# Optimization experiments

Hardware: AMD Instinct MI355X
Metric: run time of the kernel (lower is better)

The kernel has to match this reference:

```python
import jax, jax.numpy as jnp
import numpy as np

B, N, M, C, H = 256, 4096, 64, 512, 4
IN, OUT = 64, 64
EPS = 1e-8

def setup_inputs():
    key = jax.random.key(0)
    ks = jax.random.split(key, 8)
    def w(k, shape, scale=0.05):
        return jax.random.normal(k, shape, dtype=jnp.float32) * scale
    return {
        "in_data": jax.random.normal(ks[0], (B, IN), dtype=jnp.float32),
        "memory": jax.random.normal(ks[1], (B, N, M), dtype=jnp.float32),
        "h0": jnp.zeros((B, C), jnp.float32),
        "c0": jnp.zeros((B, C), jnp.float32),
        "prev_weights": jnp.zeros((2 * H, B, N), jnp.float32),
        "prev_reads": jax.random.normal(ks[2], (H, B, M), dtype=jnp.float32),
        "W_ih": w(ks[3], (4 * C, IN + H * M)),
        "b_ih": jnp.zeros((4 * C,), jnp.float32),
        "W_hh": w(ks[4], (4 * C, C)),
        "b_hh": jnp.zeros((4 * C,), jnp.float32),
        "W_out": w(ks[5], (OUT, C + H * M)),
        "b_out": jnp.zeros((OUT,), jnp.float32),
        "W_addr": w(ks[6], (2 * H, M + 6, C)),
        "b_addr": jnp.zeros((2 * H, M + 6), jnp.float32),
        "W_ea": w(ks[7], (H, 2 * M, C)),
        "b_ea": jnp.zeros((H, 2 * M), jnp.float32),
    }


def reference(in_data, memory, h0, c0, prev_weights, prev_reads,
              W_ih, b_ih, W_hh, b_hh, W_out, b_out,
              W_addr, b_addr, W_ea, b_ea):
    # ---- controller: LSTMCell over [input, prev_reads...] ----
    x = jnp.concatenate([in_data] + [prev_reads[i] for i in range(H)], axis=-1)  # [B, IN+H*M]
    gates = x @ W_ih.T + b_ih + h0 @ W_hh.T + b_hh                               # [B, 4C]
    i_g, f_g, g_g, o_g = jnp.split(gates, 4, axis=-1)
    c = jax.nn.sigmoid(f_g) * c0 + jax.nn.sigmoid(i_g) * jnp.tanh(g_g)
    h = jax.nn.sigmoid(o_g) * jnp.tanh(c)

    # ---- heads: alternate read / write, sequential over memory ----
    mem = memory
    reads = []
    for hi in range(2 * H):
        p = c @ W_addr[hi].T + b_addr[hi]                     # [B, M+6]
        k = jnp.tanh(p[:, :M])                                # key
        beta = jax.nn.softplus(p[:, M:M + 1])                 # key strength
        gate = jax.nn.sigmoid(p[:, M + 1:M + 2])              # interpolation gate
        s = jax.nn.softmax(p[:, M + 2:M + 5], axis=-1)        # shift weights (3)
        gamma = 1.0 + jax.nn.softplus(p[:, M + 5:M + 6])      # sharpening
        # content addressing: cosine similarity against all memory rows
        dot = jnp.einsum('bnm,bm->bn', mem, k)                # [B, N]
        norms = jnp.linalg.norm(mem, axis=-1) * jnp.linalg.norm(k, axis=-1, keepdims=True)
        wc = jax.nn.softmax(beta * dot / (norms + EPS), axis=-1)
        # interpolation with previous weights
        wg = gate * wc + (1.0 - gate) * prev_weights[hi]
        # circular shift convolution (shifts -1, 0, +1)
        ws = (s[:, 0:1] * jnp.roll(wg, 1, axis=-1)
              + s[:, 1:2] * wg
              + s[:, 2:3] * jnp.roll(wg, -1, axis=-1))
        # sharpening
        wp = ws ** gamma
        w = wp / (jnp.sum(wp, axis=-1, keepdims=True) + EPS)
        if hi % 2 == 0:  # read head
            reads.append(jnp.einsum('bn,bnm->bm', w, mem))
        else:            # write head: erase then add
            ea = c @ W_ea[hi // 2].T + b_ea[hi // 2]          # [B, 2M]
            e = jax.nn.sigmoid(ea[:, :M])
            a = jnp.tanh(ea[:, M:])
            mem = mem * (1.0 - w[:, :, None] * e[:, None, :]) + w[:, :, None] * a[:, None, :]

    # ---- output layer over [h, reads...] ----
    state = jnp.concatenate([h] + reads, axis=-1)             # [B, C+H*M]
    return jax.nn.sigmoid(state @ W_out.T + b_out)            # [B, OUT]
```

## Files before the change

kernel.cpp:

```cpp
#include <hip/hip_runtime.h>
#include <math.h>

#define EPSF 1e-8f

__device__ __forceinline__ float sigf(float x) { return 1.0f / (1.0f + expf(-x)); }
__device__ __forceinline__ float softplusf(float x) { return x > 20.0f ? x : log1pf(expf(x)); }

__global__ void pack_x_kernel(const float* __restrict__ in_data,
                              const float* __restrict__ prev_reads,
                              const float* __restrict__ h0,
                              float* __restrict__ X) {
  int idx = blockIdx.x * 256 + threadIdx.x;
  if (idx >= 256 * 832) return;
  int b = idx / 832, t = idx % 832;
  float v;
  if (t < 64) v = in_data[b * 64 + t];
  else if (t < 320) { int i = (t - 64) >> 6, m = (t - 64) & 63; v = prev_reads[((size_t)i * 256 + b) * 64 + m]; }
  else v = h0[b * 512 + (t - 320)];
  X[idx] = v;
}

__global__ __launch_bounds__(256) void gemm_gates_kernel(
    const float* __restrict__ X, const float* __restrict__ W_ih,
    const float* __restrict__ W_hh, const float* __restrict__ b_ih,
    const float* __restrict__ b_hh, float* __restrict__ gates) {
  __shared__ float As[16][33];
  __shared__ float Ws[16][65];
  int tid = threadIdx.x, tx = tid & 15, ty = tid >> 4;
  int row0 = blockIdx.y * 32, col0 = blockIdx.x * 64;
  float acc[2][4] = {{0,0,0,0},{0,0,0,0}};
  for (int k0 = 0; k0 < 832; k0 += 16) {
    const float* Wp; int kw, KW;
    if (k0 < 320) { Wp = W_ih; kw = k0; KW = 320; }
    else          { Wp = W_hh; kw = k0 - 320; KW = 512; }
    for (int i = tid; i < 32 * 16; i += 256) {
      int rr = i >> 4, cc = i & 15;
      As[cc][rr] = X[(size_t)(row0 + rr) * 832 + k0 + cc];
    }
    for (int i = tid; i < 64 * 16; i += 256) {
      int rr = i >> 4, cc = i & 15;
      Ws[cc][rr] = Wp[(size_t)(col0 + rr) * KW + kw + cc];
    }
    __syncthreads();
#pragma unroll
    for (int kk = 0; kk < 16; kk++) {
      float a0 = As[kk][ty * 2 + 0], a1 = As[kk][ty * 2 + 1];
      float w0 = Ws[kk][tx * 4 + 0], w1 = Ws[kk][tx * 4 + 1];
      float w2 = Ws[kk][tx * 4 + 2], w3 = Ws[kk][tx * 4 + 3];
      acc[0][0] += a0 * w0; acc[0][1] += a0 * w1; acc[0][2] += a0 * w2; acc[0][3] += a0 * w3;
      acc[1][0] += a1 * w0; acc[1][1] += a1 * w1; acc[1][2] += a1 * w2; acc[1][3] += a1 * w3;
    }
    __syncthreads();
  }
  for (int i = 0; i < 2; i++)
    for (int j = 0; j < 4; j++) {
      int cc = col0 + tx * 4 + j;
      gates[(size_t)(row0 + ty * 2 + i) * 2048 + cc] = acc[i][j] + b_ih[cc] + b_hh[cc];
    }
}

__global__ void lstm_elem_kernel(const float* __restrict__ gates,
                                 const float* __restrict__ c0,
                                 float* __restrict__ c, float* __restrict__ h) {
  int idx = blockIdx.x * 256 + threadIdx.x;
  if (idx >= 256 * 512) return;
  int b = idx >> 9, u = idx & 511;
  const float* g = gates + (size_t)b * 2048;
  float ig = sigf(g[u]), fg = sigf(g[512 + u]);
  float gg = tanhf(g[1024 + u]), og = sigf(g[1536 + u]);
  float cv = fg * c0[idx] + ig * gg;
  c[idx] = cv;
  h[idx] = og * tanhf(cv);
}

__global__ __launch_bounds__(256) void gemm_heads_kernel(
    const float* __restrict__ C, const float* __restrict__ W_addr,
    const float* __restrict__ W_ea, const float* __restrict__ b_addr,
    const float* __restrict__ b_ea, float* __restrict__ p_raw) {
  __shared__ float As[16][33];
  __shared__ float Ws[16][65];
  int tid = threadIdx.x, tx = tid & 15, ty = tid >> 4;
  int row0 = blockIdx.y * 32, col0 = blockIdx.x * 64;
  float acc[2][4] = {{0,0,0,0},{0,0,0,0}};
  for (int k0 = 0; k0 < 512; k0 += 16) {
    for (int i = tid; i < 32 * 16; i += 256) {
      int rr = i >> 4, cc = i & 15;
      As[cc][rr] = C[(size_t)(row0 + rr) * 512 + k0 + cc];
    }
    for (int i = tid; i < 64 * 16; i += 256) {
      int rr = i >> 4, cc = i & 15;
      int col = col0 + rr;
      float v = 0.f;
      if (col < 560) v = W_addr[(size_t)col * 512 + k0 + cc];
      else if (col < 1072) v = W_ea[(size_t)(col - 560) * 512 + k0 + cc];
      Ws[cc][rr] = v;
    }
    __syncthreads();
#pragma unroll
    for (int kk = 0; kk < 16; kk++) {
      float a0 = As[kk][ty * 2 + 0], a1 = As[kk][ty * 2 + 1];
      float w0 = Ws[kk][tx * 4 + 0], w1 = Ws[kk][tx * 4 + 1];
      float w2 = Ws[kk][tx * 4 + 2], w3 = Ws[kk][tx * 4 + 3];
      acc[0][0] += a0 * w0; acc[0][1] += a0 * w1; acc[0][2] += a0 * w2; acc[0][3] += a0 * w3;
      acc[1][0] += a1 * w0; acc[1][1] += a1 * w1; acc[1][2] += a1 * w2; acc[1][3] += a1 * w3;
    }
    __syncthreads();
  }
  for (int i = 0; i < 2; i++)
    for (int j = 0; j < 4; j++) {
      int col = col0 + tx * 4 + j;
      if (col < 1072) {
        float bias = col < 560 ? b_addr[col] : b_ea[col - 560];
        p_raw[(size_t)(row0 + ty * 2 + i) * 1072 + col] = acc[i][j] + bias;
      }
    }
}

__global__ void head_params_kernel(const float* __restrict__ p_raw,
    float* __restrict__ kvec, float* __restrict__ knorm,
    float* __restrict__ betav, float* __restrict__ gatev,
    float* __restrict__ sv, float* __restrict__ gammav,
    float* __restrict__ evec, float* __restrict__ avec) {
  int hi = blockIdx.x, b = blockIdx.y, t = threadIdx.x;
  const float* p = p_raw + (size_t)b * 1072 + hi * 70;
  if (t < 64) {
    float kvv = tanhf(p[t]);
    kvec[((size_t)hi * 256 + b) * 64 + t] = kvv;
    float s = kvv * kvv;
    for (int m = 1; m < 64; m <<= 1) s += __shfl_xor(s, m);
    if (t == 0) {
      int hb = hi * 256 + b;
      knorm[hb] = sqrtf(s);
      betav[hb] = softplusf(p[64]);
      gatev[hb] = sigf(p[65]);
      float a0 = p[66], a1 = p[67], a2 = p[68];
      float mm = fmaxf(a0, fmaxf(a1, a2));
      float e0 = expf(a0 - mm), e1 = expf(a1 - mm), e2 = expf(a2 - mm);
      float es = e0 + e1 + e2;
      sv[hb * 3 + 0] = e0 / es; sv[hb * 3 + 1] = e1 / es; sv[hb * 3 + 2] = e2 / es;
      gammav[hb] = 1.0f + softplusf(p[69]);
    }
  } else if ((hi & 1) && hi < 7) {
    int wj = hi >> 1, t2 = t - 64;
    const float* ea = p_raw + (size_t)b * 1072 + 560 + wj * 128;
    evec[((size_t)wj * 256 + b) * 64 + t2] = sigf(ea[t2]);
    avec[((size_t)wj * 256 + b) * 64 + t2] = tanhf(ea[64 + t2]);
  }
}

template<int NW, int NKEYS, int READ_MODE>
__global__ __launch_bounds__(256) void pass_kernel(
    const float* __restrict__ mem, const float* __restrict__ kvec,
    int keyA, int keyB, const float* __restrict__ w_all,
    const float* __restrict__ evec, const float* __restrict__ avec,
    int rw_head, float* __restrict__ dot_a, float* __restrict__ dot_b,
    float* __restrict__ normr, float* __restrict__ read_out) {
  const int BB = 256, NN = 4096;
  int b = blockIdx.y;
  int n0 = blockIdx.x * 256;
  int tid = threadIdx.x;
  int wv = tid >> 6, lane = tid & 63;
  int q = lane & 15, r = lane >> 4;
  size_t bo = (size_t)b * NN;

  float4 kA = make_float4(0,0,0,0), kB = make_float4(0,0,0,0);
  if (NKEYS >= 1) kA = *(const float4*)(kvec + ((size_t)keyA * BB + b) * 64 + q * 4);
  if (NKEYS >= 2) kB = *(const float4*)(kvec + ((size_t)keyB * BB + b) * 64 + q * 4);
  float4 ev[3], av[3];
  const float* wrow[3];
  const int whead[3] = {1, 3, 5};
#pragma unroll
  for (int j = 0; j < NW; j++) {
    ev[j] = *(const float4*)(evec + ((size_t)j * BB + b) * 64 + q * 4);
    av[j] = *(const float4*)(avec + ((size_t)j * BB + b) * 64 + q * 4);
    wrow[j] = w_all + ((size_t)whead[j] * BB + b) * NN;
  }
  const float* rwrow = READ_MODE ? (w_all + ((size_t)rw_head * BB + b) * NN) : nullptr;

  __shared__ float sdA[256], sdB[256], snm[256];
  __shared__ float sred[4][16][4];

  const float4* m4 = (const float4*)mem;
  size_t base = (bo + n0 + (size_t)wv * 64) * 16 + lane;

  float rx = 0.f, ry = 0.f, rz = 0.f, rw_ = 0.f;
#pragma unroll 4
  for (int t = 0; t < 16; t++) {
    int nl = wv * 64 + t * 4 + r;
    int n = n0 + nl;
    float4 v = m4[base + (size_t)t * 64];
    float vx = v.x, vy = v.y, vz = v.z, vw = v.w;
#pragma unroll
    for (int j = 0; j < NW; j++) {
      if (READ_MODE == 1 && j == NW - 1) {
        float rwt = rwrow[n];
        rx += rwt * vx; ry += rwt * vy; rz += rwt * vz; rw_ += rwt * vw;
      }
      float wj = wrow[j][n];
      vx = vx * (1.f - wj * ev[j].x) + wj * av[j].x;
      vy = vy * (1.f - wj * ev[j].y) + wj * av[j].y;
      vz = vz * (1.f - wj * ev[j].z) + wj * av[j].z;
      vw = vw * (1.f - wj * ev[j].w) + wj * av[j].w;
    }
    if (READ_MODE == 2) {
      float rwt = rwrow[n];
      rx += rwt * vx; ry += rwt * vy; rz += rwt * vz; rw_ += rwt * vw;
    }
    if (NKEYS >= 1) {
      float dA = vx * kA.x + vy * kA.y + vz * kA.z + vw * kA.w;
      float nm = vx * vx + vy * vy + vz * vz + vw * vw;
      float dB = 0.f;
      if (NKEYS >= 2) dB = vx * kB.x + vy * kB.y + vz * kB.z + vw * kB.w;
#pragma unroll
      for (int m = 1; m < 16; m <<= 1) {
        dA += __shfl_xor(dA, m);
        nm += __shfl_xor(nm, m);
        if (NKEYS >= 2) dB += __shfl_xor(dB, m);
      }
      if (q == 0) {
        sdA[nl] = dA; snm[nl] = sqrtf(nm);
        if (NKEYS >= 2) sdB[nl] = dB;
      }
    }
  }
  if (READ_MODE) {
#pragma unroll
    for (int m = 16; m < 64; m <<= 1) {
      rx += __shfl_xor(rx, m); ry += __shfl_xor(ry, m);
      rz += __shfl_xor(rz, m); rw_ += __shfl_xor(rw_, m);
    }
    if (r == 0) { sred[wv][q][0] = rx; sred[wv][q][1] = ry; sred[wv][q][2] = rz; sred[wv][q][3] = rw_; }
  }
  __syncthreads();
  if (NKEYS >= 1) {
    dot_a[bo + n0 + tid] = sdA[tid];
    normr[bo + n0 + tid] = snm[tid];
    if (NKEYS >= 2) dot_b[bo + n0 + tid] = sdB[tid];
  }
  if (READ_MODE && tid < 64) {
    int qq = tid >> 2, cc = tid & 3;
    float s = sred[0][qq][cc] + sred[1][qq][cc] + sred[2][qq][cc] + sred[3][qq][cc];
    atomicAdd(&read_out[b * 64 + qq * 4 + cc], s);
  }
}

__global__ __launch_bounds__(256) void chain_kernel(
    const float* __restrict__ dot_a, const float* __restrict__ dot_b,
    const float* __restrict__ normr, const float* __restrict__ knorm,
    const float* __restrict__ betav, const float* __restrict__ gatev,
    const float* __restrict__ sv, const float* __restrict__ gammav,
    const float* __restrict__ prev_w, float* __restrict__ w_all,
    int head_base) {
  const int NN = 4096, BB = 256;
  int which = blockIdx.x, b = blockIdx.y;
  int head = head_base + which;
  const float* dp = which ? dot_b : dot_a;
  size_t bo = (size_t)b * NN;
  __shared__ float wg[4096];
  __shared__ float redm[4], reds[4], reds2[4];
  int tid = threadIdx.x;
  int lane = tid & 63, wv = tid >> 6;
  int hb = head * BB + b;
  float kn = knorm[hb], be = betav[hb], ga = gatev[hb], gm = gammav[hb];
  float s0 = sv[hb * 3 + 0], s1 = sv[hb * 3 + 1], s2 = sv[hb * 3 + 2];

  float sc[16];
  float mx = -1e30f;
#pragma unroll
  for (int i = 0; i < 16; i++) {
    int n = tid + i * 256;
    float d = dp[bo + n], rn = normr[bo + n];
    sc[i] = be * d / (rn * kn + EPSF);
    mx = fmaxf(mx, sc[i]);
  }
  for (int m = 1; m < 64; m <<= 1) mx = fmaxf(mx, __shfl_xor(mx, m));
  if (lane == 0) redm[wv] = mx;
  __syncthreads();
  mx = fmaxf(fmaxf(redm[0], redm[1]), fmaxf(redm[2], redm[3]));
  float sum = 0.f;
#pragma unroll
  for (int i = 0; i < 16; i++) { sc[i] = expf(sc[i] - mx); sum += sc[i]; }
  for (int m = 1; m < 64; m <<= 1) sum += __shfl_xor(sum, m);
  if (lane == 0) reds[wv] = sum;
  __syncthreads();
  sum = reds[0] + reds[1] + reds[2] + reds[3];
  float inv = 1.0f / sum;
  const float* pw = prev_w + (size_t)head * BB * NN + bo;
#pragma unroll
  for (int i = 0; i < 16; i++) {
    int n = tid + i * 256;
    wg[n] = ga * (sc[i] * inv) + (1.f - ga) * pw[n];
  }
  __syncthreads();
  float wp[16];
  float sum2 = 0.f;
#pragma unroll
  for (int i = 0; i < 16; i++) {
    int n = tid + i * 256;
    float wsv = s0 * wg[(n + NN - 1) & (NN - 1)] + s1 * wg[n] + s2 * wg[(n + 1) & (NN - 1)];
    wp[i] = powf(wsv, gm);
    sum2 += wp[i];
  }
  for (int m = 1; m < 64; m <<= 1) sum2 += __shfl_xor(sum2, m);
  if (lane == 0) reds2[wv] = sum2;
  __syncthreads();
  sum2 = reds2[0] + reds2[1] + reds2[2] + reds2[3];
  float invs = 1.0f / (sum2 + EPSF);
  float* wo = w_all + (size_t)head * BB * NN + bo;
#pragma unroll
  for (int i = 0; i < 16; i++) wo[tid + i * 256] = wp[i] * invs;
}

__global__ void pack_state_kernel(const float* __restrict__ h,
                                  const float* __restrict__ reads,
                                  float* __restrict__ state) {
  int idx = blockIdx.x * 256 + threadIdx.x;
  if (idx >= 256 * 768) return;
  int b = idx / 768, t = idx % 768;
  float v;
  if (t < 512) v = h[b * 512 + t];
  else { int slot = (t - 512) >> 6, m = (t - 512) & 63; v = reads[((size_t)slot * 256 + b) * 64 + m]; }
  state[idx] = v;
}

__global__ __launch_bounds__(256) void gemm_out_kernel(
    const float* __restrict__ state, const float* __restrict__ W_out,
    const float* __restrict__ b_out, float* __restrict__ out) {
  __shared__ float As[16][33];
  __shared__ float Ws[16][65];
  int tid = threadIdx.x, tx = tid & 15, ty = tid >> 4;
  int row0 = blockIdx.y * 32;
  float acc[2][4] = {{0,0,0,0},{0,0,0,0}};
  for (int k0 = 0; k0 < 768; k0 += 16) {
    for (int i = tid; i < 32 * 16; i += 256) {
      int rr = i >> 4, cc = i & 15;
      As[cc][rr] = state[(size_t)(row0 + rr) * 768 + k0 + cc];
    }
    for (int i = tid; i < 64 * 16; i += 256) {
      int rr = i >> 4, cc = i & 15;
      Ws[cc][rr] = W_out[(size_t)rr * 768 + k0 + cc];
    }
    __syncthreads();
#pragma unroll
    for (int kk = 0; kk < 16; kk++) {
      float a0 = As[kk][ty * 2 + 0], a1 = As[kk][ty * 2 + 1];
      float w0 = Ws[kk][tx * 4 + 0], w1 = Ws[kk][tx * 4 + 1];
      float w2 = Ws[kk][tx * 4 + 2], w3 = Ws[kk][tx * 4 + 3];
      acc[0][0] += a0 * w0; acc[0][1] += a0 * w1; acc[0][2] += a0 * w2; acc[0][3] += a0 * w3;
      acc[1][0] += a1 * w0; acc[1][1] += a1 * w1; acc[1][2] += a1 * w2; acc[1][3] += a1 * w3;
    }
    __syncthreads();
  }
  for (int i = 0; i < 2; i++)
    for (int j = 0; j < 4; j++) {
      int cc = tx * 4 + j;
      out[(size_t)(row0 + ty * 2 + i) * 64 + cc] = sigf(acc[i][j] + b_out[cc]);
    }
}

extern "C" void kernel_launch(void* const* d_in, const int* in_sizes, int n_in,
                              void* d_out, int out_size, void* d_ws, size_t ws_size,
                              hipStream_t stream) {
  const float* in_data = (const float*)d_in[0];
  const float* memory  = (const float*)d_in[1];
  const float* h0      = (const float*)d_in[2];
  const float* c0      = (const float*)d_in[3];
  const float* prev_w  = (const float*)d_in[4];
  const float* prev_r  = (const float*)d_in[5];
  const float* W_ih    = (const float*)d_in[6];
  const float* b_ih    = (const float*)d_in[7];
  const float* W_hh    = (const float*)d_in[8];
  const float* b_hh    = (const float*)d_in[9];
  const float* W_out   = (const float*)d_in[10];
  const float* b_out   = (const float*)d_in[11];
  const float* W_addr  = (const float*)d_in[12];
  const float* b_addr  = (const float*)d_in[13];
  const float* W_ea    = (const float*)d_in[14];
  const float* b_ea    = (const float*)d_in[15];
  float* out = (float*)d_out;
  (void)in_sizes; (void)n_in; (void)out_size; (void)ws_size;

  float* ws = (float*)d_ws;
  size_t off = 0;
  auto alloc = [&](size_t n) { float* p = ws + off; off += (n + 63) & ~(size_t)63; return p; };
  float* X      = alloc(256 * 832);
  float* gates  = alloc(256 * 2048);
  float* cbuf   = alloc(256 * 512);
  float* hbuf   = alloc(256 * 512);
  float* p_raw  = alloc(256 * 1072);
  float* kvec   = alloc(8 * 256 * 64);
  float* knorm  = alloc(8 * 256);
  float* betav  = alloc(8 * 256);
  float* gatev  = alloc(8 * 256);
  float* sv     = alloc(8 * 256 * 3);
  float* gammav = alloc(8 * 256);
  float* evec   = alloc(3 * 256 * 64);
  float* avec   = alloc(3 * 256 * 64);
  float* dot_a  = alloc((size_t)256 * 4096);
  float* dot_b  = alloc((size_t)256 * 4096);
  float* normr  = alloc((size_t)256 * 4096);
  float* w_all  = alloc((size_t)7 * 256 * 4096);
  float* reads  = alloc(4 * 256 * 64);
  float* state  = alloc(256 * 768);

  hipMemsetAsync(reads, 0, 4 * 256 * 64 * sizeof(float), stream);

  pack_x_kernel<<<(256 * 832 + 255) / 256, 256, 0, stream>>>(in_data, prev_r, h0, X);
  gemm_gates_kernel<<<dim3(32, 8), 256, 0, stream>>>(X, W_ih, W_hh, b_ih, b_hh, gates);
  lstm_elem_kernel<<<(256 * 512 + 255) / 256, 256, 0, stream>>>(gates, c0, cbuf, hbuf);
  gemm_heads_kernel<<<dim3(17, 8), 256, 0, stream>>>(cbuf, W_addr, W_ea, b_addr, b_ea, p_raw);
  head_params_kernel<<<dim3(8, 256), 128, 0, stream>>>(p_raw, kvec, knorm, betav, gatev, sv, gammav, evec, avec);

  dim3 pgrid(16, 256);
  pass_kernel<0, 2, 0><<<pgrid, 256, 0, stream>>>(memory, kvec, 0, 1, w_all, evec, avec, 0,
                                                  dot_a, dot_b, normr, reads);
  chain_kernel<<<dim3(2, 256), 256, 0, stream>>>(dot_a, dot_b, normr, knorm, betav, gatev, sv, gammav, prev_w, w_all, 0);
  pass_kernel<1, 2, 1><<<pgrid, 256, 0, stream>>>(memory, kvec, 2, 3, w_all, evec, avec, 0,
                                                  dot_a, dot_b, normr, reads + 0 * 256 * 64);
  chain_kernel<<<dim3(2, 256), 256, 0, stream>>>(dot_a, dot_b, normr, knorm, betav, gatev, sv, gammav, prev_w, w_all, 2);
  pass_kernel<2, 2, 1><<<pgrid, 256, 0, stream>>>(memory, kvec, 4, 5, w_all, evec, avec, 2,
                                                  dot_a, dot_b, normr, reads + 1 * 256 * 64);
  chain_kernel<<<dim3(2, 256), 256, 0, stream>>>(dot_a, dot_b, normr, knorm, betav, gatev, sv, gammav, prev_w, w_all, 4);
  pass_kernel<3, 1, 1><<<pgrid, 256, 0, stream>>>(memory, kvec, 6, 6, w_all, evec, avec, 4,
                                                  dot_a, dot_b, normr, reads + 2 * 256 * 64);
  chain_kernel<<<dim3(1, 256), 256, 0, stream>>>(dot_a, dot_b, normr, knorm, betav, gatev, sv, gammav, prev_w, w_all, 6);
  pass_kernel<3, 0, 2><<<pgrid, 256, 0, stream>>>(memory, kvec, 0, 0, w_all, evec, avec, 6,
                                                  dot_a, dot_b, normr, reads + 3 * 256 * 64);

  pack_state_kernel<<<(256 * 768 + 255) / 256, 256, 0, stream>>>(hbuf, reads, state);
  gemm_out_kernel<<<dim3(1, 8), 256, 0, stream>>>(state, W_out, b_out, out);
}
```

Measured before the change: 982.4 us.

## Expand write-head updates algebraically to cut full memory passes from five to three

The content-addressing dot products and norms after a write are expanded algebraically in terms of the original memory and precomputed key/erase/add combinations. Two memory passes compute all the needed projections at once, and the chain kernel reassembles dot and squared norm per row from those planes and the current write weight. This cuts the number of full 256MB memory sweeps from five to three. In exchange it writes and reads many extra B×N planes (20 instead of 3), and the expanded norm may lose precision through cancellation, which is clamped at zero.

```diff
diff --git a/kernel.cpp b/kernel.cpp
--- a/kernel.cpp
+++ b/kernel.cpp
@@ -2,9 +2,13 @@
 #include <math.h>
 
 #define EPSF 1e-8f
+#define PLANE ((size_t)256 * 4096)
 
 __device__ __forceinline__ float sigf(float x) { return 1.0f / (1.0f + expf(-x)); }
 __device__ __forceinline__ float softplusf(float x) { return x > 20.0f ? x : log1pf(expf(x)); }
+__device__ __forceinline__ float dot4(float4 a, float4 b) {
+  return a.x * b.x + a.y * b.y + a.z * b.z + a.w * b.w;
+}
 
 __global__ void pack_x_kernel(const float* __restrict__ in_data,
                               const float* __restrict__ prev_reads,
@@ -148,113 +152,237 @@
   }
 }
 
-template<int NW, int NKEYS, int READ_MODE>
-__global__ __launch_bounds__(256) void pass_kernel(
-    const float* __restrict__ mem, const float* __restrict__ kvec,
-    int keyA, int keyB, const float* __restrict__ w_all,
+__global__ void combo_kernel(const float* __restrict__ kvec,
+                             const float* __restrict__ evec,
+                             const float* __restrict__ avec,
+                             float* __restrict__ combo, float* __restrict__ scal) {
+  int b = blockIdx.x, m = threadIdx.x;
+  size_t bm = (size_t)b * 64 + m;
+  float k0 = kvec[0 * 16384 + bm], k1 = kvec[1 * 16384 + bm];
+  float k2 = kvec[2 * 16384 + bm], k3 = kvec[3 * 16384 + bm];
+  float k4 = kvec[4 * 16384 + bm], k5 = kvec[5 * 16384 + bm];
+  float k6 = kvec[6 * 16384 + bm];
+  float e1 = evec[0 * 16384 + bm], a1 = avec[0 * 16384 + bm];
+  float e3 = evec[1 * 16384 + bm], a3 = avec[1 * 16384 + bm];
+  float e5 = evec[2 * 16384 + bm], a5 = avec[2 * 16384 + bm];
+  combo[0 * 16384 + bm] = k0;  combo[1 * 16384 + bm] = k1;
+  combo[2 * 16384 + bm] = k2;  combo[3 * 16384 + bm] = e1 * k2;
+  combo[4 * 16384 + bm] = k3;  combo[5 * 16384 + bm] = e1 * k3;
+  combo[6 * 16384 + bm] = a1;  combo[7 * 16384 + bm] = e1 * a1;
+  combo[8 * 16384 + bm] = e1;  combo[9 * 16384 + bm] = e1 * e1;
+  combo[10 * 16384 + bm] = k4; combo[11 * 16384 + bm] = k5;
+  combo[12 * 16384 + bm] = k6; combo[13 * 16384 + bm] = e5 * k6;
+  combo[14 * 16384 + bm] = a5; combo[15 * 16384 + bm] = e5 * a5;
+  combo[16 * 16384 + bm] = e5; combo[17 * 16384 + bm] = e5 * e5;
+  combo[18 * 16384 + bm] = e3; combo[19 * 16384 + bm] = a3;
+  float s0 = a1 * k2, s1 = a1 * k3, s2 = a1 * a1, s3 = a5 * k6, s4 = a5 * a5;
+#pragma unroll
+  for (int d = 1; d < 64; d <<= 1) {
+    s0 += __shfl_xor(s0, d); s1 += __shfl_xor(s1, d); s2 += __shfl_xor(s2, d);
+    s3 += __shfl_xor(s3, d); s4 += __shfl_xor(s4, d);
+  }
+  if (m == 0) {
+    scal[b * 8 + 0] = s0; scal[b * 8 + 1] = s1; scal[b * 8 + 2] = s2;
+    scal[b * 8 + 3] = s3; scal[b * 8 + 4] = s4;
+  }
+}
+
+#define LDC(j, q) (*(const float4*)(cb + (size_t)(j) * 16384 + (q) * 4))
+
+__global__ __launch_bounds__(256) void dotpass1_kernel(
+    const float* __restrict__ mem, const float* __restrict__ combo,
+    float* __restrict__ P1) {
+  extern __shared__ float4 tile[];
+  const int NN = 4096;
+  int b = blockIdx.y, n0 = blockIdx.x * 256, tid = threadIdx.x;
+  const float4* m4 = (const float4*)mem + ((size_t)b * NN + n0) * 16;
+#pragma unroll
+  for (int i = 0; i < 16; i++) {
+    int L = tid + i * 256, r = L >> 4, q = L & 15;
+    tile[r * 16 + (q ^ (r & 15))] = m4[L];
+  }
+  __syncthreads();
+  const float* cb = combo + (size_t)b * 64;
+  float d0=0,d1=0,d2=0,d3=0,d4=0,d5=0,d6=0,d7=0,s0=0,s1=0,s2=0;
+#pragma unroll
+  for (int q = 0; q < 16; q++) {
+    float4 v = tile[tid * 16 + (q ^ (tid & 15))];
+    float4 sq = make_float4(v.x*v.x, v.y*v.y, v.z*v.z, v.w*v.w);
+    d0 += dot4(v, LDC(0, q)); d1 += dot4(v, LDC(1, q));
+    d2 += dot4(v, LDC(2, q)); d3 += dot4(v, LDC(3, q));
+    d4 += dot4(v, LDC(4, q)); d5 += dot4(v, LDC(5, q));
+    d6 += dot4(v, LDC(6, q)); d7 += dot4(v, LDC(7, q));
+    s0 += sq.x + sq.y + sq.z + sq.w;
+    s1 += dot4(sq, LDC(8, q)); s2 += dot4(sq, LDC(9, q));
+  }
+  size_t o = (size_t)b * NN + n0 + tid;
+  P1[0*PLANE+o]=d0; P1[1*PLANE+o]=d1; P1[2*PLANE+o]=d2; P1[3*PLANE+o]=d3;
+  P1[4*PLANE+o]=d4; P1[5*PLANE+o]=d5; P1[6*PLANE+o]=d6; P1[7*PLANE+o]=d7;
+  P1[8*PLANE+o]=s0; P1[9*PLANE+o]=s1; P1[10*PLANE+o]=s2;
+}
+
+__global__ __launch_bounds__(256) void dotpass2_kernel(
+    const float* __restrict__ mem, const float* __restrict__ combo,
+    const float* __restrict__ w_all, float* __restrict__ P2,
+    float* __restrict__ reads) {
+  extern __shared__ float4 tile[];
+  const int NN = 4096;
+  int b = blockIdx.y, n0 = blockIdx.x * 256, tid = threadIdx.x;
+  size_t bo = (size_t)b * NN;
+  const float4* m4 = (const float4*)mem + (bo + n0) * 16;
+#pragma unroll
+  for (int i = 0; i < 16; i++) {
+    int L = tid + i * 256, r = L >> 4, q = L & 15;
+    tile[r * 16 + (q ^ (r & 15))] = m4[L];
+  }
+  __syncthreads();
+  const float* cb = combo + (size_t)b * 64;
+  float u1 = w_all[1 * PLANE + bo + n0 + tid];
+  float u3 = w_all[3 * PLANE + bo + n0 + tid];
+  float t0=0,t1=0,t2=0,t3=0,t4=0,t5=0,r0=0,r1=0,r2=0;
+#pragma unroll
+  for (int q = 0; q < 16; q++) {
+    float4 v = tile[tid * 16 + (q ^ (tid & 15))];
+    float4 e1 = LDC(8, q), aa1 = LDC(6, q), e3 = LDC(18, q), aa3 = LDC(19, q);
+    float4 m1, m2;
+    m1.x = v.x * (1.f - u1 * e1.x) + u1 * aa1.x;
+    m1.y = v.y * (1.f - u1 * e1.y) + u1 * aa1.y;
+    m1.z = v.z * (1.f - u1 * e1.z) + u1 * aa1.z;
+    m1.w = v.w * (1.f - u1 * e1.w) + u1 * aa1.w;
+    m2.x = m1.x * (1.f - u3 * e3.x) + u3 * aa3.x;
+    m2.y = m1.y * (1.f - u3 * e3.y) + u3 * aa3.y;
+    m2.z = m1.z * (1.f - u3 * e3.z) + u3 * aa3.z;
+    m2.w = m1.w * (1.f - u3 * e3.w) + u3 * aa3.w;
+    float4 sq = make_float4(m2.x*m2.x, m2.y*m2.y, m2.z*m2.z, m2.w*m2.w);
+    t0 += dot4(m2, LDC(10, q)); t1 += dot4(m2, LDC(11, q));
+    t2 += dot4(m2, LDC(12, q)); t3 += dot4(m2, LDC(13, q));
+    t4 += dot4(m2, LDC(14, q)); t5 += dot4(m2, LDC(15, q));
+    r0 += sq.x + sq.y + sq.z + sq.w;
+    r1 += dot4(sq, LDC(16, q)); r2 += dot4(sq, LDC(17, q));
+  }
+  size_t o = bo + n0 + tid;
+  P2[0*PLANE+o]=t0; P2[1*PLANE+o]=t1; P2[2*PLANE+o]=t2; P2[3*PLANE+o]=t3;
+  P2[4*PLANE+o]=t4; P2[5*PLANE+o]=t5; P2[6*PLANE+o]=r0; P2[7*PLANE+o]=r1; P2[8*PLANE+o]=r2;
+
+  __shared__ float sredA[4][16][4];
+  __shared__ float sredB[4][16][4];
+  int wv = tid >> 6, lane = tid & 63, q = lane & 15, rl = lane >> 4;
+  float4 e1q = LDC(8, q), a1q = LDC(6, q);
+  const float* w0r = w_all + 0 * PLANE + bo;
+  const float* w1r = w_all + 1 * PLANE + bo;
+  const float* w2r = w_all + 2 * PLANE + bo;
+  float ax=0, ay=0, az=0, aw=0, bx=0, by=0, bz=0, bw=0;
+#pragma unroll 4
+  for (int t = 0; t < 16; t++) {
+    int nl = wv * 64 + t * 4 + rl, n = n0 + nl;
+    float4 v = tile[nl * 16 + (q ^ (nl & 15))];
+    float w0v = w0r[n], u1b = w1r[n], w2v = w2r[n];
+    ax += w0v * v.x; ay += w0v * v.y; az += w0v * v.z; aw += w0v * v.w;
+    float m1x = v.x * (1.f - u1b * e1q.x) + u1b * a1q.x;
+    float m1y = v.y * (1.f - u1b * e1q.y) + u1b * a1q.y;
+    float m1z = v.z * (1.f - u1b * e1q.z) + u1b * a1q.z;
+    float m1w = v.w * (1.f - u1b * e1q.w) + u1b * a1q.w;
+    bx += w2v * m1x; by += w2v * m1y; bz += w2v * m1z; bw += w2v * m1w;
+  }
+#pragma unroll
+  for (int m = 16; m < 64; m <<= 1) {
+    ax += __shfl_xor(ax, m); ay += __shfl_xor(ay, m); az += __shfl_xor(az, m); aw += __shfl_xor(aw, m);
+    bx += __shfl_xor(bx, m); by += __shfl_xor(by, m); bz += __shfl_xor(bz, m); bw += __shfl_xor(bw, m);
+  }
+  if (rl == 0) {
+    sredA[wv][q][0]=ax; sredA[wv][q][1]=ay; sredA[wv][q][2]=az; sredA[wv][q][3]=aw;
+    sredB[wv][q][0]=bx; sredB[wv][q][1]=by; sredB[wv][q][2]=bz; sredB[wv][q][3]=bw;
+  }
+  __syncthreads();
+  if (tid < 64) {
+    int qq = tid >> 2, cc = tid & 3;
+    float sA = sredA[0][qq][cc] + sredA[1][qq][cc] + sredA[2][qq][cc] + sredA[3][qq][cc];
+    float sB = sredB[0][qq][cc] + sredB[1][qq][cc] + sredB[2][qq][cc] + sredB[3][qq][cc];
+    atomicAdd(&reads[0 * 16384 + b * 64 + qq * 4 + cc], sA);
+    atomicAdd(&reads[1 * 16384 + b * 64 + qq * 4 + cc], sB);
+  }
+}
+
+__global__ __launch_bounds__(256) void readpass_kernel(
+    const float* __restrict__ mem, const float* __restrict__ w_all,
     const float* __restrict__ evec, const float* __restrict__ avec,
-    int rw_head, float* __restrict__ dot_a, float* __restrict__ dot_b,
-    float* __restrict__ normr, float* __restrict__ read_out) {
-  const int BB = 256, NN = 4096;
-  int b = blockIdx.y;
-  int n0 = blockIdx.x * 256;
-  int tid = threadIdx.x;
-  int wv = tid >> 6, lane = tid & 63;
-  int q = lane & 15, r = lane >> 4;
+    float* __restrict__ reads) {
+  const int NN = 4096;
+  int b = blockIdx.y, n0 = blockIdx.x * 256, tid = threadIdx.x;
+  int wv = tid >> 6, lane = tid & 63, q = lane & 15, rl = lane >> 4;
   size_t bo = (size_t)b * NN;
-
-  float4 kA = make_float4(0,0,0,0), kB = make_float4(0,0,0,0);
-  if (NKEYS >= 1) kA = *(const float4*)(kvec + ((size_t)keyA * BB + b) * 64 + q * 4);
-  if (NKEYS >= 2) kB = *(const float4*)(kvec + ((size_t)keyB * BB + b) * 64 + q * 4);
-  float4 ev[3], av[3];
-  const float* wrow[3];
-  const int whead[3] = {1, 3, 5};
-#pragma unroll
-  for (int j = 0; j < NW; j++) {
-    ev[j] = *(const float4*)(evec + ((size_t)j * BB + b) * 64 + q * 4);
-    av[j] = *(const float4*)(avec + ((size_t)j * BB + b) * 64 + q * 4);
-    wrow[j] = w_all + ((size_t)whead[j] * BB + b) * NN;
-  }
-  const float* rwrow = READ_MODE ? (w_all + ((size_t)rw_head * BB + b) * NN) : nullptr;
-
-  __shared__ float sdA[256], sdB[256], snm[256];
-  __shared__ float sred[4][16][4];
-
+  float4 e1 = *(const float4*)(evec + 0 * 16384 + b * 64 + q * 4);
+  float4 a1 = *(const float4*)(avec + 0 * 16384 + b * 64 + q * 4);
+  float4 e3 = *(const float4*)(evec + 1 * 16384 + b * 64 + q * 4);
+  float4 a3 = *(const float4*)(avec + 1 * 16384 + b * 64 + q * 4);
+  float4 e5 = *(const float4*)(evec + 2 * 16384 + b * 64 + q * 4);
+  float4 a5 = *(const float4*)(avec + 2 * 16384 + b * 64 + q * 4);
+  const float* w1r = w_all + 1 * PLANE + bo;
+  const float* w3r = w_all + 3 * PLANE + bo;
+  const float* w5r = w_all + 5 * PLANE + bo;
+  const float* w4r = w_all + 4 * PLANE + bo;
+  const float* w6r = w_all + 6 * PLANE + bo;
+  __shared__ float sredA[4][16][4];
+  __shared__ float sredB[4][16][4];
   const float4* m4 = (const float4*)mem;
   size_t base = (bo + n0 + (size_t)wv * 64) * 16 + lane;
-
-  float rx = 0.f, ry = 0.f, rz = 0.f, rw_ = 0.f;
+  float ax=0, ay=0, az=0, aw=0, bx=0, by=0, bz=0, bw=0;
 #pragma unroll 4
   for (int t = 0; t < 16; t++) {
-    int nl = wv * 64 + t * 4 + r;
-    int n = n0 + nl;
+    int nl = wv * 64 + t * 4 + rl, n = n0 + nl;
     float4 v = m4[base + (size_t)t * 64];
-    float vx = v.x, vy = v.y, vz = v.z, vw = v.w;
-#pragma unroll
-    for (int j = 0; j < NW; j++) {
-      if (READ_MODE == 1 && j == NW - 1) {
-        float rwt = rwrow[n];
-        rx += rwt * vx; ry += rwt * vy; rz += rwt * vz; rw_ += rwt * vw;
-      }
-      float wj = wrow[j][n];
-      vx = vx * (1.f - wj * ev[j].x) + wj * av[j].x;
-      vy = vy * (1.f - wj * ev[j].y) + wj * av[j].y;
-      vz = vz * (1.f - wj * ev[j].z) + wj * av[j].z;
-      vw = vw * (1.f - wj * ev[j].w) + wj * av[j].w;
-    }
-    if (READ_MODE == 2) {
-      float rwt = rwrow[n];
-      rx += rwt * vx; ry += rwt * vy; rz += rwt * vz; rw_ += rwt * vw;
-    }
-    if (NKEYS >= 1) {
-      float dA = vx * kA.x + vy * kA.y + vz * kA.z + vw * kA.w;
-      float nm = vx * vx + vy * vy + vz * vz + vw * vw;
-      float dB = 0.f;
-      if (NKEYS >= 2) dB = vx * kB.x + vy * kB.y + vz * kB.z + vw * kB.w;
-#pragma unroll
-      for (int m = 1; m < 16; m <<= 1) {
-        dA += __shfl_xor(dA, m);
-        nm += __shfl_xor(nm, m);
-        if (NKEYS >= 2) dB += __shfl_xor(dB, m);
-      }
-      if (q == 0) {
-        sdA[nl] = dA; snm[nl] = sqrtf(nm);
-        if (NKEYS >= 2) sdB[nl] = dB;
-      }
-    }
-  }
-  if (READ_MODE) {
-#pragma unroll
-    for (int m = 16; m < 64; m <<= 1) {
-      rx += __shfl_xor(rx, m); ry += __shfl_xor(ry, m);
-      rz += __shfl_xor(rz, m); rw_ += __shfl_xor(rw_, m);
-    }
-    if (r == 0) { sred[wv][q][0] = rx; sred[wv][q][1] = ry; sred[wv][q][2] = rz; sred[wv][q][3] = rw_; }
-  }
-  __syncthreads();
-  if (NKEYS >= 1) {
-    dot_a[bo + n0 + tid] = sdA[tid];
-    normr[bo + n0 + tid] = snm[tid];
-    if (NKEYS >= 2) dot_b[bo + n0 + tid] = sdB[tid];
-  }
-  if (READ_MODE && tid < 64) {
+    float u1 = w1r[n], u3 = w3r[n], u5 = w5r[n], w4v = w4r[n], w6v = w6r[n];
+    float m1x = v.x * (1.f - u1 * e1.x) + u1 * a1.x;
+    float m1y = v.y * (1.f - u1 * e1.y) + u1 * a1.y;
+    float m1z = v.z * (1.f - u1 * e1.z) + u1 * a1.z;
+    float m1w = v.w * (1.f - u1 * e1.w) + u1 * a1.w;
+    float m2x = m1x * (1.f - u3 * e3.x) + u3 * a3.x;
+    float m2y = m1y * (1.f - u3 * e3.y) + u3 * a3.y;
+    float m2z = m1z * (1.f - u3 * e3.z) + u3 * a3.z;
+    float m2w = m1w * (1.f - u3 * e3.w) + u3 * a3.w;
+    ax += w4v * m2x; ay += w4v * m2y; az += w4v * m2z; aw += w4v * m2w;
+    float m3x = m2x * (1.f - u5 * e5.x) + u5 * a5.x;
+    float m3y = m2y * (1.f - u5 * e5.y) + u5 * a5.y;
+    float m3z = m2z * (1.f - u5 * e5.z) + u5 * a5.z;
+    float m3w = m2w * (1.f - u5 * e5.w) + u5 * a5.w;
+    bx += w6v * m3x; by += w6v * m3y; bz += w6v * m3z; bw += w6v * m3w;
+  }
+#pragma unroll
+  for (int m = 16; m < 64; m <<= 1) {
+    ax += __shfl_xor(ax, m); ay += __shfl_xor(ay, m); az += __shfl_xor(az, m); aw += __shfl_xor(aw, m);
+    bx += __shfl_xor(bx, m); by += __shfl_xor(by, m); bz += __shfl_xor(bz, m); bw += __shfl_xor(bw, m);
+  }
+  if (rl == 0) {
+    sredA[wv][q][0]=ax; sredA[wv][q][1]=ay; sredA[wv][q][2]=az; sredA[wv][q][3]=aw;
+    sredB[wv][q][0]=bx; sredB[wv][q][1]=by; sredB[wv][q][2]=bz; sredB[wv][q][3]=bw;
+  }
+  __syncthreads();
+  if (tid < 64) {
     int qq = tid >> 2, cc = tid & 3;
-    float s = sred[0][qq][cc] + sred[1][qq][cc] + sred[2][qq][cc] + sred[3][qq][cc];
-    atomicAdd(&read_out[b * 64 + qq * 4 + cc], s);
-  }
-}
-
+    float sA = sredA[0][qq][cc] + sredA[1][qq][cc] + sredA[2][qq][cc] + sredA[3][qq][cc];
+    float sB = sredB[0][qq][cc] + sredB[1][qq][cc] + sredB[2][qq][cc] + sredB[3][qq][cc];
+    atomicAdd(&reads[2 * 16384 + b * 64 + qq * 4 + cc], sA);
+    atomicAdd(&reads[3 * 16384 + b * 64 + qq * 4 + cc], sB);
+  }
+}
+
+template<int MODE>
 __global__ __launch_bounds__(256) void chain_kernel(
-    const float* __restrict__ dot_a, const float* __restrict__ dot_b,
-    const float* __restrict__ normr, const float* __restrict__ knorm,
-    const float* __restrict__ betav, const float* __restrict__ gatev,
-    const float* __restrict__ sv, const float* __restrict__ gammav,
-    const float* __restrict__ prev_w, float* __restrict__ w_all,
-    int head_base) {
+    const float* __restrict__ DaA, const float* __restrict__ DaB,
+    const float* __restrict__ DbA, const float* __restrict__ DbB,
+    const float* __restrict__ D6, const float* __restrict__ D7,
+    const float* __restrict__ S0, const float* __restrict__ S1,
+    const float* __restrict__ S2, const float* __restrict__ uplane,
+    const float* __restrict__ scal, int cak_slot, int caa_slot,
+    const float* __restrict__ knorm, const float* __restrict__ betav,
+    const float* __restrict__ gatev, const float* __restrict__ sv,
+    const float* __restrict__ gammav, const float* __restrict__ prev_w,
+    float* __restrict__ w_all, int head_base) {
   const int NN = 4096, BB = 256;
   int which = blockIdx.x, b = blockIdx.y;
   int head = head_base + which;
-  const float* dp = which ? dot_b : dot_a;
+  const float* Da = which ? DaB : DaA;
+  const float* Db = which ? DbB : DbA;
   size_t bo = (size_t)b * NN;
   __shared__ float wg[4096];
   __shared__ float redm[4], reds[4], reds2[4];
@@ -263,14 +391,26 @@
   int hb = head * BB + b;
   float kn = knorm[hb], be = betav[hb], ga = gatev[hb], gm = gammav[hb];
   float s0 = sv[hb * 3 + 0], s1 = sv[hb * 3 + 1], s2 = sv[hb * 3 + 2];
+  float cak = 0.f, caa = 0.f;
+  if (MODE) { cak = scal[b * 8 + cak_slot + which]; caa = scal[b * 8 + caa_slot]; }
 
   float sc[16];
   float mx = -1e30f;
 #pragma unroll
   for (int i = 0; i < 16; i++) {
     int n = tid + i * 256;
-    float d = dp[bo + n], rn = normr[bo + n];
-    sc[i] = be * d / (rn * kn + EPSF);
+    float d, nn2;
+    if (MODE) {
+      float u = uplane[bo + n];
+      d = Da[bo + n] - u * Db[bo + n] + u * cak;
+      nn2 = S0[bo + n] - 2.f * u * S1[bo + n] + u * u * S2[bo + n]
+          + 2.f * u * D6[bo + n] - 2.f * u * u * D7[bo + n] + u * u * caa;
+      nn2 = fmaxf(nn2, 0.f);
+    } else {
+      d = Da[bo + n];
+      nn2 = S0[bo + n];
+    }
+    sc[i] = be * d / (sqrtf(nn2) * kn + EPSF);
     mx = fmaxf(mx, sc[i]);
   }
   for (int m = 1; m < 64; m <<= 1) mx = fmaxf(mx, __shfl_xor(mx, m));
@@ -396,10 +536,11 @@
   float* gammav = alloc(8 * 256);
   float* evec   = alloc(3 * 256 * 64);
   float* avec   = alloc(3 * 256 * 64);
-  float* dot_a  = alloc((size_t)256 * 4096);
-  float* dot_b  = alloc((size_t)256 * 4096);
-  float* normr  = alloc((size_t)256 * 4096);
-  float* w_all  = alloc((size_t)7 * 256 * 4096);
+  float* combo  = alloc(20 * 256 * 64);
+  float* scal   = alloc(256 * 8);
+  float* P1     = alloc(11 * PLANE);
+  float* P2     = alloc(9 * PLANE);
+  float* w_all  = alloc(7 * PLANE);
   float* reads  = alloc(4 * 256 * 64);
   float* state  = alloc(256 * 768);
 
@@ -410,22 +551,32 @@
   lstm_elem_kernel<<<(256 * 512 + 255) / 256, 256, 0, stream>>>(gates, c0, cbuf, hbuf);
   gemm_heads_kernel<<<dim3(17, 8), 256, 0, stream>>>(cbuf, W_addr, W_ea, b_addr, b_ea, p_raw);
   head_params_kernel<<<dim3(8, 256), 128, 0, stream>>>(p_raw, kvec, knorm, betav, gatev, sv, gammav, evec, avec);
+  combo_kernel<<<256, 64, 0, stream>>>(kvec, evec, avec, combo, scal);
 
   dim3 pgrid(16, 256);
-  pass_kernel<0, 2, 0><<<pgrid, 256, 0, stream>>>(memory, kvec, 0, 1, w_all, evec, avec, 0,
-                                                  dot_a, dot_b, normr, reads);
-  chain_kernel<<<dim3(2, 256), 256, 0, stream>>>(dot_a, dot_b, normr, knorm, betav, gatev, sv, gammav, prev_w, w_all, 0);
-  pass_kernel<1, 2, 1><<<pgrid, 256, 0, stream>>>(memory, kvec, 2, 3, w_all, evec, avec, 0,
-                                                  dot_a, dot_b, normr, reads + 0 * 256 * 64);
-  chain_kernel<<<dim3(2, 256), 256, 0, stream>>>(dot_a, dot_b, normr, knorm, betav, gatev, sv, gammav, prev_w, w_all, 2);
-  pass_kernel<2, 2, 1><<<pgrid, 256, 0, stream>>>(memory, kvec, 4, 5, w_all, evec, avec, 2,
-                                                  dot_a, dot_b, normr, reads + 1 * 256 * 64);
-  chain_kernel<<<dim3(2, 256), 256, 0, stream>>>(dot_a, dot_b, normr, knorm, betav, gatev, sv, gammav, prev_w, w_all, 4);
-  pass_kernel<3, 1, 1><<<pgrid, 256, 0, stream>>>(memory, kvec, 6, 6, w_all, evec, avec, 4,
-                                                  dot_a, dot_b, normr, reads + 2 * 256 * 64);
-  chain_kernel<<<dim3(1, 256), 256, 0, stream>>>(dot_a, dot_b, normr, knorm, betav, gatev, sv, gammav, prev_w, w_all, 6);
-  pass_kernel<3, 0, 2><<<pgrid, 256, 0, stream>>>(memory, kvec, 0, 0, w_all, evec, avec, 6,
-                                                  dot_a, dot_b, normr, reads + 3 * 256 * 64);
+  dotpass1_kernel<<<pgrid, 256, 65536, stream>>>(memory, combo, P1);
+  chain_kernel<0><<<dim3(2, 256), 256, 0, stream>>>(
+      P1 + 0 * PLANE, P1 + 1 * PLANE, nullptr, nullptr, nullptr, nullptr,
+      P1 + 8 * PLANE, nullptr, nullptr, nullptr, scal, 0, 0,
+      knorm, betav, gatev, sv, gammav, prev_w, w_all, 0);
+  chain_kernel<1><<<dim3(2, 256), 256, 0, stream>>>(
+      P1 + 2 * PLANE, P1 + 4 * PLANE, P1 + 3 * PLANE, P1 + 5 * PLANE,
+      P1 + 6 * PLANE, P1 + 7 * PLANE,
+      P1 + 8 * PLANE, P1 + 9 * PLANE, P1 + 10 * PLANE, w_all + 1 * PLANE,
+      scal, 0, 2,
+      knorm, betav, gatev, sv, gammav, prev_w, w_all, 2);
+  dotpass2_kernel<<<pgrid, 256, 65536, stream>>>(memory, combo, w_all, P2, reads);
+  chain_kernel<0><<<dim3(2, 256), 256, 0, stream>>>(
+      P2 + 0 * PLANE, P2 + 1 * PLANE, nullptr, nullptr, nullptr, nullptr,
+      P2 + 6 * PLANE, nullptr, nullptr, nullptr, scal, 0, 0,
+      knorm, betav, gatev, sv, gammav, prev_w, w_all, 4);
+  chain_kernel<1><<<dim3(1, 256), 256, 0, stream>>>(
+      P2 + 2 * PLANE, nullptr, P2 + 3 * PLANE, nullptr,
+      P2 + 4 * PLANE, P2 + 5 * PLANE,
+      P2 + 6 * PLANE, P2 + 7 * PLANE, P2 + 8 * PLANE, w_all + 5 * PLANE,
+      scal, 3, 4,
+      knorm, betav, gatev, sv, gammav, prev_w, w_all, 6);
+  readpass_kernel<<<pgrid, 256, 0, stream>>>(memory, w_all, evec, avec, reads);
 
   pack_state_kernel<<<(256 * 768 + 255) / 256, 256, 0, stream>>>(hbuf, reads, state);
   gemm_out_kernel<<<dim3(1, 8), 256, 0, stream>>>(state, W_out, b_out, out);
```

Measured after the change: 1.012 ms. +3.0%, slower.
